# Performance work log

Measured on AMD Instinct MI355X. Metric: run time of the kernel, lower is better.

The kernel has to match this reference:

```python
import jax, jax.numpy as jnp
import numpy as np

N_TOTAL = 65536      # total nodes = NUM_GRAPHS * PER_GRAPH
NUM_GRAPHS = 1024
PER_GRAPH = 64       # num_nodes in module (per-graph)
E = 1048576          # edges, avg degree 16
IN_C = 128
HID_C = 128
OUT_C = 128
T = 8                # num_time_intervals
FC_OUT = T * PER_GRAPH * PER_GRAPH * 2  # 65536


def setup_inputs() -> dict:
    key = jax.random.key(0)
    ks = jax.random.split(key, 8)
    x = jax.random.normal(ks[0], (N_TOTAL, IN_C), dtype=jnp.float32)
    edge_index = jax.random.randint(ks[1], (2, E), 0, N_TOTAL, dtype=jnp.int64)
    batch = (jnp.arange(N_TOTAL, dtype=jnp.int64) // PER_GRAPH)  # graph id per node
    s = 0.05
    W1 = jax.random.normal(ks[2], (IN_C, HID_C), dtype=jnp.float32) * s
    b1 = jnp.zeros((HID_C,), dtype=jnp.float32)
    W2 = jax.random.normal(ks[3], (HID_C, OUT_C), dtype=jnp.float32) * s
    b2 = jnp.zeros((OUT_C,), dtype=jnp.float32)
    Wfc = jax.random.normal(ks[4], (OUT_C, FC_OUT), dtype=jnp.float32) * s
    bfc = jnp.zeros((FC_OUT,), dtype=jnp.float32)
    return {"x": x, "edge_index": edge_index, "batch": batch,
            "W1": W1, "b1": b1, "W2": W2, "b2": b2, "Wfc": Wfc, "bfc": bfc}


def reference(x, edge_index, batch, W1, b1, W2, b2, Wfc, bfc):
    n = x.shape[0]
    loop = jnp.arange(n)
    # GCNConv default: add self loops, symmetric normalization
    src = jnp.concatenate([edge_index[0], loop])
    dst = jnp.concatenate([edge_index[1], loop])
    deg = jax.ops.segment_sum(jnp.ones_like(dst, dtype=x.dtype), dst, num_segments=n)
    dinv = jnp.where(deg > 0, jax.lax.rsqrt(deg), 0.0)
    enorm = dinv[src] * dinv[dst]  # [E+n]

    def gcn(h, W, b):
        hw = h @ W                             # [n, C_out]
        msg = hw[src] * enorm[:, None]         # gather + per-edge scale
        return jax.ops.segment_sum(msg, dst, num_segments=n) + b

    h = jax.nn.relu(gcn(x, W1, b1))
    h = jax.nn.relu(gcn(h, W2, b2))

    # global_mean_pool over batch segments
    sums = jax.ops.segment_sum(h, batch, num_segments=NUM_GRAPHS)
    cnt = jax.ops.segment_sum(jnp.ones((n, 1), h.dtype), batch, num_segments=NUM_GRAPHS)
    pooled = sums / jnp.maximum(cnt, 1.0)

    out = pooled @ Wfc + bfc                   # [NUM_GRAPHS, FC_OUT]
    return out.reshape(-1, T, PER_GRAPH, PER_GRAPH * 2)
```

## Files before the change

### kernel.cpp

```cpp
#include <hip/hip_runtime.h>
#include <hip/hip_bf16.h>
#include <cstdint>

#define NODES  65536
#define CH     128
#define NGRAPH 1024
#define PGRAPH 64
#define FCO    65536

typedef __bf16 bf16x8 __attribute__((ext_vector_type(8)));
typedef __bf16 bf16x4 __attribute__((ext_vector_type(4)));
typedef float  f32x4  __attribute__((ext_vector_type(4)));

__device__ __forceinline__ float bflo(unsigned u){ return __uint_as_float(u << 16); }
__device__ __forceinline__ float bfhi(unsigned u){ return __uint_as_float(u & 0xffff0000u); }


__global__ void k_zero2(int* __restrict__ a, int* __restrict__ b){
  const int i = blockIdx.x*256 + threadIdx.x;
  ((int4*)a)[i] = make_int4(0,0,0,0);
  ((int4*)b)[i] = make_int4(0,0,0,0);
}

__global__ void k_degree(const int* __restrict__ dst, int* __restrict__ deg, int E){
  int e = blockIdx.x*256 + threadIdx.x;
  if (e < E) atomicAdd(&deg[dst[e]], 1);
}

__global__ void k_dinv(const int* __restrict__ deg, float* __restrict__ dinv){
  int i = blockIdx.x*256 + threadIdx.x;
  dinv[i] = 1.0f / sqrtf((float)(deg[i] + 1));
}

__global__ void k_scan1(const int* __restrict__ deg, int* __restrict__ excl,
                        int* __restrict__ bsums){
  __shared__ int tmp[256];
  const int t = threadIdx.x;
  const int gid = blockIdx.x*256 + t;
  const int v = deg[gid];
  tmp[t] = v;
  __syncthreads();
  #pragma unroll
  for (int off = 1; off < 256; off <<= 1){
    int x = (t >= off) ? tmp[t-off] : 0;
    __syncthreads();
    tmp[t] += x;
    __syncthreads();
  }
  excl[gid] = tmp[t] - v;
  if (t == 255) bsums[blockIdx.x] = tmp[255];
}

__global__ void k_scan2(int* __restrict__ bsums){
  __shared__ int tmp[256];
  const int t = threadIdx.x;
  const int v = bsums[t];
  tmp[t] = v;
  __syncthreads();
  #pragma unroll
  for (int off = 1; off < 256; off <<= 1){
    int x = (t >= off) ? tmp[t-off] : 0;
    __syncthreads();
    tmp[t] += x;
    __syncthreads();
  }
  bsums[t] = tmp[t] - v;
}

__global__ void k_scan3(int* __restrict__ cstart, const int* __restrict__ bsums, int E){
  const int gid = blockIdx.x*256 + threadIdx.x;
  cstart[gid] += bsums[blockIdx.x];
  if (gid == 0) cstart[NODES] = E;
}

__global__ void k_scatter(const int* __restrict__ src, const int* __restrict__ dst,
                          const int* __restrict__ cstart, int* __restrict__ cursor,
                          int* __restrict__ ssrc, int E){
  int e = blockIdx.x*256 + threadIdx.x;
  if (e >= E) return;
  const int d = dst[e];
  const int p = cstart[d] + atomicAdd(&cursor[d], 1);
  ssrc[p] = src[e];
}

template<int ACT>
__global__ __launch_bounds__(256)
void k_gemm128(const float* __restrict__ A, const float* __restrict__ W,
               const float* __restrict__ bias, __bf16* __restrict__ Cout){
  __shared__ float As[128][36];
  __shared__ float Ws[32][160];
  const int t  = threadIdx.x;
  const int r0 = blockIdx.x * 128;
  const int q  = t & 3;
  const int rp = t >> 2;

  float acc0[32], acc1[32];
  #pragma unroll
  for (int j = 0; j < 32; ++j){ acc0[j] = 0.f; acc1[j] = 0.f; }

  for (int kc = 0; kc < 128; kc += 32){
    {
      const int row = t >> 1, u = t & 1;
      const float* ap = A + (size_t)(r0+row)*CH + kc + u*16;
      float* asp = &As[row][u*16];
      #pragma unroll
      for (int i = 0; i < 4; ++i){
        float4 v = *(const float4*)(ap + 4*i);
        if (ACT){
          const float4 bb = *(const float4*)(bias + kc + u*16 + 4*i);
          v.x = fmaxf(v.x+bb.x, 0.f); v.y = fmaxf(v.y+bb.y, 0.f);
          v.z = fmaxf(v.z+bb.z, 0.f); v.w = fmaxf(v.w+bb.w, 0.f);
        }
        *(float4*)(asp + 4*i) = v;
      }
    }
    {
      const int kk = t >> 3, u = t & 7;
      const float* wp = W + (size_t)(kc+kk)*CH + u*16;
      float* wsp = &Ws[kk][(u>>1)*40 + (u&1)*16];
      #pragma unroll
      for (int i = 0; i < 4; ++i)
        *(float4*)(wsp + 4*i) = *(const float4*)(wp + 4*i);
    }
    __syncthreads();

    #pragma unroll
    for (int kk4 = 0; kk4 < 8; ++kk4){
      const float4 a0 = *(const float4*)&As[rp][kk4*4];
      const float4 a1 = *(const float4*)&As[rp+64][kk4*4];
      const float a0f[4] = {a0.x, a0.y, a0.z, a0.w};
      const float a1f[4] = {a1.x, a1.y, a1.z, a1.w};
      #pragma unroll
      for (int kk = 0; kk < 4; ++kk){
        const float av0 = a0f[kk], av1 = a1f[kk];
        #pragma unroll
        for (int j4 = 0; j4 < 8; ++j4){
          const float4 w = *(const float4*)&Ws[kk4*4+kk][q*40 + j4*4];
          acc0[j4*4+0] = fmaf(av0, w.x, acc0[j4*4+0]);
          acc0[j4*4+1] = fmaf(av0, w.y, acc0[j4*4+1]);
          acc0[j4*4+2] = fmaf(av0, w.z, acc0[j4*4+2]);
          acc0[j4*4+3] = fmaf(av0, w.w, acc0[j4*4+3]);
          acc1[j4*4+0] = fmaf(av1, w.x, acc1[j4*4+0]);
          acc1[j4*4+1] = fmaf(av1, w.y, acc1[j4*4+1]);
          acc1[j4*4+2] = fmaf(av1, w.z, acc1[j4*4+2]);
          acc1[j4*4+3] = fmaf(av1, w.w, acc1[j4*4+3]);
        }
      }
    }
    __syncthreads();
  }

  __bf16* c0 = Cout + (size_t)(r0+rp)*CH    + q*32;
  __bf16* c1 = Cout + (size_t)(r0+rp+64)*CH + q*32;
  #pragma unroll
  for (int j4 = 0; j4 < 8; ++j4){
    bf16x4 v0, v1;
    #pragma unroll
    for (int e = 0; e < 4; ++e){ v0[e] = (__bf16)acc0[j4*4+e]; v1[e] = (__bf16)acc1[j4*4+e]; }
    *(bf16x4*)(c0 + j4*4) = v0;
    *(bf16x4*)(c1 + j4*4) = v1;
  }
}

__global__ __launch_bounds__(256)
void k_agg(const __bf16* __restrict__ hw, const float* __restrict__ dinv,
           const int* __restrict__ start, const int* __restrict__ srcs,
           float* __restrict__ outp){
  const int wave = threadIdx.x >> 6, l = threadIdx.x & 63;
  const int i = blockIdx.x*4 + wave;
  const int c = l*2;
  const float di = dinv[i];
  const unsigned hs = *(const unsigned*)&hw[(size_t)i*CH + c];
  float ax = di * bflo(hs), ay = di * bfhi(hs);

  int p = start[i];
  const int p1 = start[i+1];
  for (; p + 7 < p1; p += 8){
    int s[8];
    #pragma unroll
    for (int u = 0; u < 8; ++u) s[u] = srcs[p+u];
    float w[8]; unsigned r[8];
    #pragma unroll
    for (int u = 0; u < 8; ++u){
      w[u] = dinv[s[u]];
      r[u] = *(const unsigned*)&hw[(size_t)s[u]*CH + c];
    }
    #pragma unroll
    for (int u = 0; u < 8; ++u){ ax += w[u]*bflo(r[u]); ay += w[u]*bfhi(r[u]); }
  }
  for (; p < p1; ++p){
    const int s = srcs[p];
    const float w = dinv[s];
    const unsigned r = *(const unsigned*)&hw[(size_t)s*CH + c];
    ax += w*bflo(r); ay += w*bfhi(r);
  }
  float2 o; o.x = di*ax; o.y = di*ay;
  *(float2*)&outp[(size_t)i*CH + c] = o;
}

__global__ void k_pool(const float* __restrict__ h, const float* __restrict__ b2,
                       __bf16* __restrict__ phi, __bf16* __restrict__ plo){
  const int g = blockIdx.x, c = threadIdx.x;
  const float bb = b2[c];
  float acc = 0.f;
  const float* hp = h + (size_t)g*PGRAPH*CH + c;
  #pragma unroll 4
  for (int i = 0; i < PGRAPH; ++i) acc += fmaxf(hp[i*CH] + bb, 0.f);
  const float v = acc * (1.0f/64.0f);
  const __bf16 hv = (__bf16)v;
  phi[g*CH + c] = hv;
  plo[g*CH + c] = (__bf16)(v - (float)hv);
}

__global__ __launch_bounds__(256)
void k_cvt_wfc(const float* __restrict__ Wfc, __bf16* __restrict__ wth,
               __bf16* __restrict__ wtl){
  __shared__ float ls[128][65];
  const int t  = threadIdx.x;
  const int c0 = blockIdx.x*64;

  #pragma unroll 8
  for (int it = 0; it < 32; ++it){
    const int row = it*4 + (t>>6);
    ls[row][t&63] = Wfc[(size_t)row*FCO + c0 + (t&63)];
  }
  __syncthreads();

  const int col = t>>2, q = t&3;
  const int tg  = (c0>>4) + (col>>4);
  const int lc  = col & 15;
  __bf16* dh = wth + (size_t)tg*2048 + q*512 + lc*8;
  __bf16* dl = wtl + (size_t)tg*2048 + q*512 + lc*8;
  #pragma unroll
  for (int i = 0; i < 4; ++i){
    bf16x8 h8, l8;
    #pragma unroll
    for (int j = 0; j < 8; ++j){
      const float v = ls[q*32 + i*8 + j][col];
      const __bf16 hv = (__bf16)v;
      h8[j] = hv;
      l8[j] = (__bf16)(v - (float)hv);
    }
    *(bf16x8*)(dh + i*128) = h8;
    *(bf16x8*)(dl + i*128) = l8;
  }
}

__global__ __launch_bounds__(256, 4)
void k_fc_mfma(const __bf16* __restrict__ phi, const __bf16* __restrict__ plo,
               const __bf16* __restrict__ wth, const __bf16* __restrict__ wtl,
               const float* __restrict__ bfc, float* __restrict__ out){
  const int t    = threadIdx.x;
  const int lane = t & 63, wave = t >> 6;
  const int lc   = lane & 15, kq = lane >> 4;
  const int g0   = blockIdx.y*32;
  const int c0w  = blockIdx.x*2048 + wave*512;

  bf16x8 ah[2][4], al[2][4];
  #pragma unroll
  for (int gt = 0; gt < 2; ++gt){
    const __bf16* pa = phi + (size_t)(g0 + gt*16 + lc)*CH + kq*8;
    const __bf16* pb = plo + (size_t)(g0 + gt*16 + lc)*CH + kq*8;
    #pragma unroll
    for (int kk = 0; kk < 4; ++kk){
      ah[gt][kk] = *(const bf16x8*)(pa + kk*32);
      al[gt][kk] = *(const bf16x8*)(pb + kk*32);
    }
  }

  const __bf16* bhp = wth + (size_t)(c0w >> 4)*2048 + lane*8;
  const __bf16* blp = wtl + (size_t)(c0w >> 4)*2048 + lane*8;
  float* o0 = out + (size_t)(g0 + lc)*FCO + c0w + kq*4;
  float* o1 = o0 + (size_t)16*FCO;
  const float* bp = bfc + c0w + kq*4;

  #pragma unroll 1
  for (int it = 0; it < 32; ++it){
    bf16x8 bh[4], bl[4];
    #pragma unroll
    for (int kk = 0; kk < 4; ++kk){
      bh[kk] = *(const bf16x8*)(bhp + kk*512);
      bl[kk] = *(const bf16x8*)(blp + kk*512);
    }
    f32x4 q0 = {0.f,0.f,0.f,0.f}, q1 = {0.f,0.f,0.f,0.f};
    #pragma unroll
    for (int kk = 0; kk < 4; ++kk){
      q0 = __builtin_amdgcn_mfma_f32_16x16x32_bf16(bh[kk], ah[0][kk], q0, 0,0,0);
      q1 = __builtin_amdgcn_mfma_f32_16x16x32_bf16(bh[kk], ah[1][kk], q1, 0,0,0);
      q0 = __builtin_amdgcn_mfma_f32_16x16x32_bf16(bl[kk], ah[0][kk], q0, 0,0,0);
      q1 = __builtin_amdgcn_mfma_f32_16x16x32_bf16(bl[kk], ah[1][kk], q1, 0,0,0);
      q0 = __builtin_amdgcn_mfma_f32_16x16x32_bf16(bh[kk], al[0][kk], q0, 0,0,0);
      q1 = __builtin_amdgcn_mfma_f32_16x16x32_bf16(bh[kk], al[1][kk], q1, 0,0,0);
    }
    const float4 b4 = *(const float4*)bp;
    float4 v;
    v.x = q0[0]+b4.x; v.y = q0[1]+b4.y; v.z = q0[2]+b4.z; v.w = q0[3]+b4.w;
    *(float4*)o0 = v;
    v.x = q1[0]+b4.x; v.y = q1[1]+b4.y; v.z = q1[2]+b4.z; v.w = q1[3]+b4.w;
    *(float4*)o1 = v;
    bhp += 2048; blp += 2048; o0 += 16; o1 += 16; bp += 16;
  }
}


extern "C" void kernel_launch(void* const* d_in, const int* in_sizes, int n_in,
                              void* d_out, int out_size, void* d_ws, size_t ws_size,
                              hipStream_t stream){
  const float* x   = (const float*)d_in[0];
  const int*   ei  = (const int*)d_in[1];
  const float* W1  = (const float*)d_in[3];
  const float* b1  = (const float*)d_in[4];
  const float* W2  = (const float*)d_in[5];
  const float* b2  = (const float*)d_in[6];
  const float* Wfc = (const float*)d_in[7];
  const float* bfc = (const float*)d_in[8];
  float* out = (float*)d_out;
  const int E = in_sizes[1] / 2;

  float* bufA   = (float*)d_ws;
  float* bufB   = bufA + (size_t)NODES*CH;
  float* dinv   = bufB + (size_t)NODES*CH;
  int*   deg    = (int*)(dinv + NODES);
  int*   cstart = deg + NODES;
  int*   cursor = cstart + NODES + 256;
  int*   bsums  = cursor + NODES;
  int*   ssrc   = bsums + 256;
  __bf16* phi   = (__bf16*)(ssrc + E);
  __bf16* plo   = phi + (size_t)NGRAPH*CH;

  __bf16* hwb = (__bf16*)bufA;
  __bf16* wth = (__bf16*)bufA;
  __bf16* wtl = wth + (size_t)FCO*CH;

  const int* esrc = ei;
  const int* edst = ei + E;

  k_zero2  <<<NODES/1024,  256, 0, stream>>>(deg, cursor);
  k_degree <<<(E+255)/256, 256, 0, stream>>>(edst, deg, E);
  k_dinv   <<<NODES/256,   256, 0, stream>>>(deg, dinv);
  k_scan1  <<<NODES/256,   256, 0, stream>>>(deg, cstart, bsums);
  k_scan2  <<<1,           256, 0, stream>>>(bsums);
  k_scan3  <<<NODES/256,   256, 0, stream>>>(cstart, bsums, E);
  k_scatter<<<(E+255)/256, 256, 0, stream>>>(esrc, edst, cstart, cursor, ssrc, E);

  k_gemm128<0><<<NODES/128, 256, 0, stream>>>(x,    W1, nullptr, hwb);
  k_agg       <<<NODES/4, 256, 0, stream>>>(hwb, dinv, cstart, ssrc, bufB);
  k_gemm128<1><<<NODES/128, 256, 0, stream>>>(bufB, W2, b1,     hwb);
  k_agg       <<<NODES/4, 256, 0, stream>>>(hwb, dinv, cstart, ssrc, bufB);

  k_cvt_wfc <<<FCO/64, 256, 0, stream>>>(Wfc, wth, wtl);
  k_pool    <<<NGRAPH, CH, 0, stream>>>(bufB, b2, phi, plo);
  k_fc_mfma <<<dim3(32, NGRAPH/32), 256, 0, stream>>>(phi, plo, wth, wtl, bfc, out);
}
```

Baseline: 430.9 us.

## Fuse bias+ReLU into aggregation, store hidden as bf16, widen agg loads

The aggregation kernel now applies bias and ReLU itself and writes bf16 instead of fp32. The second GEMM and the pooling kernel therefore read bf16 input and no longer need the bias/activation step. Aggregation is also restructured so each 16-lane group handles one node with 16-byte loads, giving four nodes per wave instead of one. This halves intermediate traffic and makes the gathers wider, at the cost of extra bf16 rounding on the hidden activations.

New measurement: 415.8 us. 3.5% less time.

```diff
diff --git a/kernel.cpp b/kernel.cpp
--- a/kernel.cpp
+++ b/kernel.cpp
@@ -83,10 +83,10 @@
   ssrc[p] = src[e];
 }
 
-template<int ACT>
+template<int ABF>
 __global__ __launch_bounds__(256)
-void k_gemm128(const float* __restrict__ A, const float* __restrict__ W,
-               const float* __restrict__ bias, __bf16* __restrict__ Cout){
+void k_gemm128(const void* __restrict__ Av, const float* __restrict__ W,
+               __bf16* __restrict__ Cout){
   __shared__ float As[128][36];
   __shared__ float Ws[32][160];
   const int t  = threadIdx.x;
@@ -101,17 +101,18 @@
   for (int kc = 0; kc < 128; kc += 32){
     {
       const int row = t >> 1, u = t & 1;
-      const float* ap = A + (size_t)(r0+row)*CH + kc + u*16;
       float* asp = &As[row][u*16];
-      #pragma unroll
-      for (int i = 0; i < 4; ++i){
-        float4 v = *(const float4*)(ap + 4*i);
-        if (ACT){
-          const float4 bb = *(const float4*)(bias + kc + u*16 + 4*i);
-          v.x = fmaxf(v.x+bb.x, 0.f); v.y = fmaxf(v.y+bb.y, 0.f);
-          v.z = fmaxf(v.z+bb.z, 0.f); v.w = fmaxf(v.w+bb.w, 0.f);
-        }
-        *(float4*)(asp + 4*i) = v;
+      if (ABF){
+        const __bf16* ap = (const __bf16*)Av + (size_t)(r0+row)*CH + kc + u*16;
+        const bf16x8 v0 = *(const bf16x8*)ap;
+        const bf16x8 v1 = *(const bf16x8*)(ap + 8);
+        #pragma unroll
+        for (int j = 0; j < 8; ++j){ asp[j] = (float)v0[j]; asp[8+j] = (float)v1[j]; }
+      } else {
+        const float* ap = (const float*)Av + (size_t)(r0+row)*CH + kc + u*16;
+        #pragma unroll
+        for (int i = 0; i < 4; ++i)
+          *(float4*)(asp + 4*i) = *(const float4*)(ap + 4*i);
       }
     }
     {
@@ -165,47 +166,64 @@
 __global__ __launch_bounds__(256)
 void k_agg(const __bf16* __restrict__ hw, const float* __restrict__ dinv,
            const int* __restrict__ start, const int* __restrict__ srcs,
-           float* __restrict__ outp){
-  const int wave = threadIdx.x >> 6, l = threadIdx.x & 63;
-  const int i = blockIdx.x*4 + wave;
-  const int c = l*2;
+           const float* __restrict__ bias, __bf16* __restrict__ outp){
+  const int l = threadIdx.x & 63, wave = threadIdx.x >> 6;
+  const int n = l >> 4;
+  const int q = l & 15;
+  const int i = blockIdx.x*16 + wave*4 + n;
+  const int c = q*8;
   const float di = dinv[i];
-  const unsigned hs = *(const unsigned*)&hw[(size_t)i*CH + c];
-  float ax = di * bflo(hs), ay = di * bfhi(hs);
+
+  const uint4 hs = *(const uint4*)&hw[(size_t)i*CH + c];
+  float acc[8];
+  acc[0] = di*bflo(hs.x); acc[1] = di*bfhi(hs.x);
+  acc[2] = di*bflo(hs.y); acc[3] = di*bfhi(hs.y);
+  acc[4] = di*bflo(hs.z); acc[5] = di*bfhi(hs.z);
+  acc[6] = di*bflo(hs.w); acc[7] = di*bfhi(hs.w);
 
   int p = start[i];
   const int p1 = start[i+1];
-  for (; p + 7 < p1; p += 8){
-    int s[8];
-    #pragma unroll
-    for (int u = 0; u < 8; ++u) s[u] = srcs[p+u];
-    float w[8]; unsigned r[8];
-    #pragma unroll
-    for (int u = 0; u < 8; ++u){
-      w[u] = dinv[s[u]];
-      r[u] = *(const unsigned*)&hw[(size_t)s[u]*CH + c];
-    }
-    #pragma unroll
-    for (int u = 0; u < 8; ++u){ ax += w[u]*bflo(r[u]); ay += w[u]*bfhi(r[u]); }
+  for (; p + 3 < p1; p += 4){
+    const int s0 = srcs[p], s1 = srcs[p+1], s2 = srcs[p+2], s3 = srcs[p+3];
+    const float w0 = dinv[s0], w1 = dinv[s1], w2 = dinv[s2], w3 = dinv[s3];
+    const uint4 r0 = *(const uint4*)&hw[(size_t)s0*CH + c];
+    const uint4 r1 = *(const uint4*)&hw[(size_t)s1*CH + c];
+    const uint4 r2 = *(const uint4*)&hw[(size_t)s2*CH + c];
+    const uint4 r3 = *(const uint4*)&hw[(size_t)s3*CH + c];
+    acc[0]+=w0*bflo(r0.x); acc[1]+=w0*bfhi(r0.x); acc[2]+=w0*bflo(r0.y); acc[3]+=w0*bfhi(r0.y);
+    acc[4]+=w0*bflo(r0.z); acc[5]+=w0*bfhi(r0.z); acc[6]+=w0*bflo(r0.w); acc[7]+=w0*bfhi(r0.w);
+    acc[0]+=w1*bflo(r1.x); acc[1]+=w1*bfhi(r1.x); acc[2]+=w1*bflo(r1.y); acc[3]+=w1*bfhi(r1.y);
+    acc[4]+=w1*bflo(r1.z); acc[5]+=w1*bfhi(r1.z); acc[6]+=w1*bflo(r1.w); acc[7]+=w1*bfhi(r1.w);
+    acc[0]+=w2*bflo(r2.x); acc[1]+=w2*bfhi(r2.x); acc[2]+=w2*bflo(r2.y); acc[3]+=w2*bfhi(r2.y);
+    acc[4]+=w2*bflo(r2.z); acc[5]+=w2*bfhi(r2.z); acc[6]+=w2*bflo(r2.w); acc[7]+=w2*bfhi(r2.w);
+    acc[0]+=w3*bflo(r3.x); acc[1]+=w3*bfhi(r3.x); acc[2]+=w3*bflo(r3.y); acc[3]+=w3*bfhi(r3.y);
+    acc[4]+=w3*bflo(r3.z); acc[5]+=w3*bfhi(r3.z); acc[6]+=w3*bflo(r3.w); acc[7]+=w3*bfhi(r3.w);
   }
   for (; p < p1; ++p){
     const int s = srcs[p];
     const float w = dinv[s];
-    const unsigned r = *(const unsigned*)&hw[(size_t)s*CH + c];
-    ax += w*bflo(r); ay += w*bfhi(r);
-  }
-  float2 o; o.x = di*ax; o.y = di*ay;
-  *(float2*)&outp[(size_t)i*CH + c] = o;
-}
-
-__global__ void k_pool(const float* __restrict__ h, const float* __restrict__ b2,
+    const uint4 r = *(const uint4*)&hw[(size_t)s*CH + c];
+    acc[0]+=w*bflo(r.x); acc[1]+=w*bfhi(r.x); acc[2]+=w*bflo(r.y); acc[3]+=w*bfhi(r.y);
+    acc[4]+=w*bflo(r.z); acc[5]+=w*bfhi(r.z); acc[6]+=w*bflo(r.w); acc[7]+=w*bfhi(r.w);
+  }
+
+  const float4 b0 = *(const float4*)&bias[c];
+  const float4 b1 = *(const float4*)&bias[c+4];
+  const float bb[8] = {b0.x,b0.y,b0.z,b0.w,b1.x,b1.y,b1.z,b1.w};
+  bf16x8 o;
+  #pragma unroll
+  for (int k = 0; k < 8; ++k)
+    o[k] = (__bf16)fmaxf(di*acc[k] + bb[k], 0.f);
+  *(bf16x8*)&outp[(size_t)i*CH + c] = o;
+}
+
+__global__ void k_pool(const __bf16* __restrict__ h,
                        __bf16* __restrict__ phi, __bf16* __restrict__ plo){
   const int g = blockIdx.x, c = threadIdx.x;
-  const float bb = b2[c];
   float acc = 0.f;
-  const float* hp = h + (size_t)g*PGRAPH*CH + c;
+  const __bf16* hp = h + (size_t)g*PGRAPH*CH + c;
   #pragma unroll 4
-  for (int i = 0; i < PGRAPH; ++i) acc += fmaxf(hp[i*CH] + bb, 0.f);
+  for (int i = 0; i < PGRAPH; ++i) acc += (float)hp[i*CH];
   const float v = acc * (1.0f/64.0f);
   const __bf16 hv = (__bf16)v;
   phi[g*CH + c] = hv;
@@ -329,6 +347,7 @@
   __bf16* plo   = phi + (size_t)NGRAPH*CH;
 
   __bf16* hwb = (__bf16*)bufA;
+  __bf16* hbb = (__bf16*)bufB;
   __bf16* wth = (__bf16*)bufA;
   __bf16* wtl = wth + (size_t)FCO*CH;
 
@@ -343,12 +362,11 @@
   k_scan3  <<<NODES/256,   256, 0, stream>>>(cstart, bsums, E);
   k_scatter<<<(E+255)/256, 256, 0, stream>>>(esrc, edst, cstart, cursor, ssrc, E);
 
-  k_gemm128<0><<<NODES/128, 256, 0, stream>>>(x,    W1, nullptr, hwb);
-  k_agg       <<<NODES/4, 256, 0, stream>>>(hwb, dinv, cstart, ssrc, bufB);
-  k_gemm128<1><<<NODES/128, 256, 0, stream>>>(bufB, W2, b1,     hwb);
-  k_agg       <<<NODES/4, 256, 0, stream>>>(hwb, dinv, cstart, ssrc, bufB);
-
+  k_gemm128<0><<<NODES/128, 256, 0, stream>>>(x,   W1, hwb);
+  k_agg       <<<NODES/16, 256, 0, stream>>>(hwb, dinv, cstart, ssrc, b1, hbb);
+  k_gemm128<1><<<NODES/128, 256, 0, stream>>>(hbb, W2, hwb);
+  k_agg       <<<NODES/16, 256, 0, stream>>>(hwb, dinv, cstart, ssrc, b2, hbb);
   k_cvt_wfc <<<FCO/64, 256, 0, stream>>>(Wfc, wth, wtl);
-  k_pool    <<<NGRAPH, CH, 0, stream>>>(bufB, b2, phi, plo);
+  k_pool    <<<NGRAPH, CH, 0, stream>>>(hbb, phi, plo);
   k_fc_mfma <<<dim3(32, NGRAPH/32), 256, 0, stream>>>(phi, plo, wth, wtl, bfc, out);
 }
```
